# Optimization experiments

Measured on AMD Instinct MI355X. Metric: run time of the kernel, lower is better.

The kernel has to match this reference:

```python
import jax, jax.numpy as jnp
import numpy as np

B, N, C, K = 16, 2000, 4, 8
EPS = 1e-5


def setup_inputs() -> dict:
    key = jax.random.key(0)
    ks = jax.random.split(key, 10)
    def p(k, shape, s=0.1):
        return jax.random.normal(k, shape, jnp.float32) * s
    return {
        "data": jax.random.normal(ks[0], (B, 1, N, C), jnp.float32),
        "x": jax.random.normal(ks[1], (B, 1, N, 4), jnp.float32),
        "w1a": p(ks[2], (128, C)), "b1a": jnp.zeros((128,), jnp.float32),
        "w1b": p(ks[3], (128, 128)), "b1b": jnp.zeros((128,), jnp.float32),
        "w2": p(ks[4], (128, 2 * C + 2)), "b2": jnp.zeros((128,), jnp.float32),
        "res_wa": p(ks[5], (4, 128, 128)), "res_ba": jnp.zeros((4, 128), jnp.float32),
        "res_wb": p(ks[6], (4, 128, 128)), "res_bb": jnp.zeros((4, 128), jnp.float32),
        "wl": p(ks[7], (1, 128)), "bl": jnp.zeros((1,), jnp.float32),
    }


def conv1x1(t, w, b):
    # t: [B, Cin, H, W], w: [Cout, Cin]
    return jnp.einsum('bchw,oc->bohw', t, w) + b[None, :, None, None]


def bn(t):
    # training-mode BatchNorm2d, gamma=1 beta=0 (default init)
    m = jnp.mean(t, axis=(0, 2, 3), keepdims=True)
    v = jnp.var(t, axis=(0, 2, 3), keepdims=True)
    return (t - m) * jax.lax.rsqrt(v + EPS)


def instn(t):
    # InstanceNorm2d, affine=False
    m = jnp.mean(t, axis=(2, 3), keepdims=True)
    v = jnp.var(t, axis=(2, 3), keepdims=True)
    return (t - m) * jax.lax.rsqrt(v + EPS)


def res_block(t, wa, ba, wb, bb):
    h = jax.nn.relu(bn(instn(conv1x1(t, wa, ba))))
    h = bn(instn(conv1x1(h, wb, bb)))
    return jax.nn.relu(h + t)


def knn_idx(f, k):
    # f: [B, D, N]; negative squared distance, top-(k+1), drop self
    xx = jnp.sum(f * f, axis=1)                        # [B, N]
    inner = jnp.einsum('bdn,bdm->bnm', f, f)           # [B, N, N]
    pd = 2.0 * inner - xx[:, :, None] - xx[:, None, :]
    idx = jax.lax.top_k(pd, k + 1)[1]                  # [B, N, k+1]
    return idx[:, :, 1:]


def graph_feature(f, idx):
    # f: [B, D, N], idx: [B, N, k] -> [B, 2D, N, k]
    xf = jnp.transpose(f, (0, 2, 1))                   # [B, N, D]
    nb = jax.vmap(lambda a, i: a[i])(xf, idx)          # [B, N, k, D]
    xt = xf[:, :, None, :]
    gf = jnp.concatenate([jnp.broadcast_to(xt, nb.shape), xt - nb], axis=-1)
    return jnp.transpose(gf, (0, 3, 1, 2))


def reference(data, x, w1a, b1a, w1b, b1b, w2, b2,
              res_wa, res_ba, res_wb, res_bb, wl, bl):
    n = data.shape[2]
    t = jnp.transpose(data, (0, 3, 2, 1))              # [B, C, N, 1]

    # self_attention
    h = conv1x1(t, w1a, b1a)
    h = jax.nn.relu(bn(h))
    h = conv1x1(h, w1b, b1b)[..., 0]                   # [B, 128, N]
    h = h / (jnp.linalg.norm(h, axis=1, keepdims=True) + 1e-5)
    A_rowsum = jnp.einsum('bcn,bcm->bm', h, h)         # sum_i A[i, j]
    D = (A_rowsum - 1.0) / n                           # [B, N] (eye subtraction)
    feat = jnp.concatenate(
        [t, jax.nn.relu(jnp.tanh(D))[:, None, :, None]], axis=1)  # [B, C+1, N, 1]

    f = feat[..., 0]                                   # [B, C+1, N]
    idx = knn_idx(f, K)
    g = graph_feature(f, idx)                          # [B, 2C+2, N, K]

    out = jax.nn.relu(bn(conv1x1(g, w2, b2)))          # [B, 128, N, K]
    out = jnp.max(out, axis=-1, keepdims=True)         # [B, 128, N, 1]

    for i in range(4):
        out = res_block(out, res_wa[i], res_ba[i], res_wb[i], res_bb[i])

    logit = conv1x1(out, wl, bl)[:, 0, :, 0]           # [B, N]

    # weighted 8-point
    weights = jax.nn.relu(jnp.tanh(logit))             # [B, N]
    xp = jnp.transpose(x[:, 0], (0, 2, 1))             # [B, 4, N]
    ones = jnp.ones_like(xp[:, 0])
    X = jnp.stack([xp[:, 2] * xp[:, 0], xp[:, 2] * xp[:, 1], xp[:, 2],
                   xp[:, 3] * xp[:, 0], xp[:, 3] * xp[:, 1], xp[:, 3],
                   xp[:, 0], xp[:, 1], ones], axis=1)  # [B, 9, N]
    X = jnp.transpose(X, (0, 2, 1))                    # [B, N, 9]
    XwX = jnp.einsum('bnp,bnq->bpq', X, weights[:, :, None] * X)  # [B, 9, 9]
    _, v = jnp.linalg.eigh(XwX)                        # ascending eigvals
    e_hat = v[:, :, 0]                                 # smallest-eig eigenvector
    e_hat = e_hat / jnp.linalg.norm(e_hat, axis=1, keepdims=True)

    return (D, logit, e_hat)
```

## Files before the change

kernel.cpp:

```cpp
#include <hip/hip_runtime.h>
#include <math.h>

#define BB 16
#define NN 2000
#define CH 128
#define KNN 8
#define JCH 8
#define JSZ 250

__device__ inline float wred(float v) {
    for (int off = 32; off > 0; off >>= 1) v += __shfl_down(v, off, 64);
    return v;
}

__global__ void k_conv1(const float* __restrict__ data, const float* __restrict__ w1a,
                        const float* __restrict__ b1a, float* __restrict__ c1) {
    int i = blockIdx.x * 256 + threadIdx.x;
    if (i >= BB * CH * NN) return;
    int n = i % NN;
    int rest = i / NN;
    int o = rest & 127;
    int b = rest >> 7;
    const float* dp = data + (b * NN + n) * 4;
    float acc = b1a[o];
    for (int c = 0; c < 4; ++c) acc += w1a[o * 4 + c] * dp[c];
    c1[i] = acc;
}

__global__ void k_chanstats(const float* __restrict__ src, float* __restrict__ chAB) {
    int o = blockIdx.x;
    int tid = threadIdx.x;
    float s = 0.f, ss = 0.f;
    for (int b = 0; b < BB; ++b) {
        const float* p = src + (b * CH + o) * NN;
        for (int n = tid; n < NN; n += 256) { float v = p[n]; s += v; ss += v * v; }
    }
    s = wred(s); ss = wred(ss);
    __shared__ float sh[8];
    int wid = tid >> 6, lane = tid & 63;
    if (lane == 0) { sh[wid] = s; sh[4 + wid] = ss; }
    __syncthreads();
    if (tid == 0) {
        float S0 = sh[0] + sh[1] + sh[2] + sh[3];
        float SS = sh[4] + sh[5] + sh[6] + sh[7];
        float m = S0 / (float)(BB * NN);
        float var = SS / (float)(BB * NN) - m * m;
        float a = rsqrtf(var + 1e-5f);
        chAB[o] = a;
        chAB[CH + o] = -m * a;
    }
}

__global__ __launch_bounds__(256) void k_gemm(const float* __restrict__ X, const float* __restrict__ W,
                                              const float* __restrict__ bias, float* __restrict__ Y,
                                              const float* __restrict__ ab, int mode) {
    int ot = blockIdx.x, by = blockIdx.y;
    int b = by >> 5, nt = by & 31;
    int n0 = nt * 64, o0 = ot * 64;
    int tid = threadIdx.x;
    int tx = tid & 15, ty = tid >> 4;
    __shared__ __align__(16) float Xs[32][64];
    __shared__ __align__(16) float Ws[32][68];
    float acc[4][4] = {};
    for (int jc = 0; jc < 4; ++jc) {
#pragma unroll
        for (int q = 0; q < 2; ++q) {
            int e4 = q * 256 + tid;
            int jj = e4 >> 4, nn4 = e4 & 15;
            int j = jc * 32 + jj;
            int n = n0 + nn4 * 4;
            float4 v = make_float4(0.f, 0.f, 0.f, 0.f);
            if (n < NN) {
                v = *(const float4*)&X[(b * CH + j) * NN + n];
                if (mode == 1) {
                    float a_ = ab[j], o_ = ab[CH + j];
                    v.x = fmaxf(a_ * v.x + o_, 0.f);
                    v.y = fmaxf(a_ * v.y + o_, 0.f);
                    v.z = fmaxf(a_ * v.z + o_, 0.f);
                    v.w = fmaxf(a_ * v.w + o_, 0.f);
                } else if (mode == 2) {
                    int bc = b * CH + j;
                    float a_ = ab[bc * 2], o_ = ab[bc * 2 + 1];
                    v.x = fmaxf(a_ * v.x + o_, 0.f);
                    v.y = fmaxf(a_ * v.y + o_, 0.f);
                    v.z = fmaxf(a_ * v.z + o_, 0.f);
                    v.w = fmaxf(a_ * v.w + o_, 0.f);
                }
            }
            *(float4*)&Xs[jj][nn4 * 4] = v;
        }
#pragma unroll
        for (int q = 0; q < 2; ++q) {
            int e4 = q * 256 + tid;
            int oo = e4 >> 3, jj4 = e4 & 7;
            float4 wv4 = *(const float4*)&W[(o0 + oo) * CH + jc * 32 + jj4 * 4];
            Ws[jj4 * 4 + 0][oo] = wv4.x;
            Ws[jj4 * 4 + 1][oo] = wv4.y;
            Ws[jj4 * 4 + 2][oo] = wv4.z;
            Ws[jj4 * 4 + 3][oo] = wv4.w;
        }
        __syncthreads();
        for (int jj = 0; jj < 32; ++jj) {
            float4 wv = *(const float4*)&Ws[jj][ty * 4];
            float4 xv = *(const float4*)&Xs[jj][tx * 4];
            float wva[4] = {wv.x, wv.y, wv.z, wv.w};
            float xva[4] = {xv.x, xv.y, xv.z, xv.w};
#pragma unroll
            for (int a = 0; a < 4; ++a)
#pragma unroll
                for (int bq = 0; bq < 4; ++bq) acc[a][bq] += wva[a] * xva[bq];
        }
        __syncthreads();
    }
    for (int a = 0; a < 4; ++a) {
        int o = o0 + ty * 4 + a;
        float bi = bias[o];
        for (int q = 0; q < 4; ++q) {
            int n = n0 + tx * 4 + q;
            if (n < NN) Y[(b * CH + o) * NN + n] = acc[a][q] + bi;
        }
    }
}

__global__ void k_invn(const float* __restrict__ h2, float* __restrict__ invn) {
    int b = blockIdx.x >> 3, chunk = blockIdx.x & 7;
    int n = chunk * 256 + threadIdx.x;
    if (n >= NN) return;
    float acc = 0.f;
    for (int c = 0; c < CH; ++c) { float v = h2[(b * CH + c) * NN + n]; acc += v * v; }
    invn[b * NN + n] = 1.f / (sqrtf(acc) + 1e-5f);
}

__global__ void k_S(const float* __restrict__ h2, const float* __restrict__ invn, float* __restrict__ Sv) {
    int row = blockIdx.x;
    int b = row >> 7;
    const float* p = h2 + row * NN;
    const float* iv = invn + b * NN;
    float s = 0.f;
    for (int n = threadIdx.x; n < NN; n += 256) s += p[n] * iv[n];
    s = wred(s);
    __shared__ float sh[4];
    int wid = threadIdx.x >> 6, lane = threadIdx.x & 63;
    if (lane == 0) sh[wid] = s;
    __syncthreads();
    if (threadIdx.x == 0) Sv[row] = sh[0] + sh[1] + sh[2] + sh[3];
}

__global__ void k_Df(const float* __restrict__ h2, const float* __restrict__ invn,
                     const float* __restrict__ Sv, const float* __restrict__ data,
                     float* __restrict__ outD, float* __restrict__ f5) {
    int b = blockIdx.x >> 3, chunk = blockIdx.x & 7;
    int n = chunk * 256 + threadIdx.x;
    if (n >= NN) return;
    float acc = 0.f;
    for (int c = 0; c < CH; ++c) acc += h2[(b * CH + c) * NN + n] * Sv[b * CH + c];
    float Ar = acc * invn[b * NN + n];
    float Dv = (Ar - 1.0f) / (float)NN;
    outD[b * NN + n] = Dv;
    const float* dp = data + (b * NN + n) * 4;
    for (int c = 0; c < 4; ++c) f5[(b * 5 + c) * NN + n] = dp[c];
    f5[(b * 5 + 4) * NN + n] = fmaxf(tanhf(Dv), 0.f);
}

__device__ __forceinline__ void cas_fj(float& da, int& ja, float& db, int& jb) {
    bool sw = db < da;
    float d0 = sw ? db : da;
    float d1 = sw ? da : db;
    int j0 = sw ? jb : ja;
    int j1 = sw ? ja : jb;
    da = d0; db = d1; ja = j0; jb = j1;
}

__global__ __launch_bounds__(256, 4) void k_knn_part(const float* __restrict__ f5,
                                                     float* __restrict__ pd, int* __restrict__ pj) {
    __shared__ float4 fs4[256];
    __shared__ float fs1[256];
    int jc = blockIdx.x, ic = blockIdx.y, b = blockIdx.z;
    int j0 = jc * JSZ;
    int tid = threadIdx.x;
    const float* fb = f5 + b * 5 * NN;
    if (tid < JSZ) {
        float4 v;
        v.x = fb[0 * NN + j0 + tid];
        v.y = fb[1 * NN + j0 + tid];
        v.z = fb[2 * NN + j0 + tid];
        v.w = fb[3 * NN + j0 + tid];
        fs4[tid] = v;
        fs1[tid] = fb[4 * NN + j0 + tid];
    } else {
        fs4[tid] = make_float4(1e18f, 1e18f, 1e18f, 1e18f);
        fs1[tid] = 1e18f;
    }
    __syncthreads();
    int i = ic * 256 + tid;
    if (i >= NN) return;
    float fi0 = fb[i], fi1 = fb[NN + i], fi2 = fb[2 * NN + i], fi3 = fb[3 * NN + i], fi4 = fb[4 * NN + i];
    const float DINF = __int_as_float(0x7f800000);
    float bd[8]; int bj[8];
#pragma unroll
    for (int q = 0; q < 8; ++q) { bd[q] = 1e30f; bj[q] = 0x7fffffff; }
    for (int g = 0; g < 256; g += 8) {
        float gd[8]; int gj[8];
#pragma unroll
        for (int k = 0; k < 8; ++k) {
            float4 fj = fs4[g + k];
            float f4 = fs1[g + k];
            float a0 = fi0 - fj.x, a1 = fi1 - fj.y, a2 = fi2 - fj.z, a3 = fi3 - fj.w, a4 = fi4 - f4;
            float dd = a0 * a0 + a1 * a1 + a2 * a2 + a3 * a3 + a4 * a4;
            int jj = j0 + g + k;
            gd[k] = (jj == i) ? DINF : dd;
            gj[k] = jj;
        }
        cas_fj(gd[0], gj[0], gd[1], gj[1]); cas_fj(gd[2], gj[2], gd[3], gj[3]);
        cas_fj(gd[4], gj[4], gd[5], gj[5]); cas_fj(gd[6], gj[6], gd[7], gj[7]);
        cas_fj(gd[0], gj[0], gd[2], gj[2]); cas_fj(gd[1], gj[1], gd[3], gj[3]);
        cas_fj(gd[4], gj[4], gd[6], gj[6]); cas_fj(gd[5], gj[5], gd[7], gj[7]);
        cas_fj(gd[1], gj[1], gd[2], gj[2]); cas_fj(gd[5], gj[5], gd[6], gj[6]);
        cas_fj(gd[0], gj[0], gd[4], gj[4]); cas_fj(gd[1], gj[1], gd[5], gj[5]);
        cas_fj(gd[2], gj[2], gd[6], gj[6]); cas_fj(gd[3], gj[3], gd[7], gj[7]);
        cas_fj(gd[2], gj[2], gd[4], gj[4]); cas_fj(gd[3], gj[3], gd[5], gj[5]);
        cas_fj(gd[1], gj[1], gd[2], gj[2]); cas_fj(gd[3], gj[3], gd[4], gj[4]);
        cas_fj(gd[5], gj[5], gd[6], gj[6]);
#pragma unroll
        for (int q = 0; q < 8; ++q) {
            float yd = gd[7 - q]; int yj = gj[7 - q];
            bool kp = bd[q] < yd;
            bd[q] = kp ? bd[q] : yd;
            bj[q] = kp ? bj[q] : yj;
        }
        cas_fj(bd[0], bj[0], bd[4], bj[4]); cas_fj(bd[1], bj[1], bd[5], bj[5]);
        cas_fj(bd[2], bj[2], bd[6], bj[6]); cas_fj(bd[3], bj[3], bd[7], bj[7]);
        cas_fj(bd[0], bj[0], bd[2], bj[2]); cas_fj(bd[1], bj[1], bd[3], bj[3]);
        cas_fj(bd[4], bj[4], bd[6], bj[6]); cas_fj(bd[5], bj[5], bd[7], bj[7]);
        cas_fj(bd[0], bj[0], bd[1], bj[1]); cas_fj(bd[2], bj[2], bd[3], bj[3]);
        cas_fj(bd[4], bj[4], bd[5], bj[5]); cas_fj(bd[6], bj[6], bd[7], bj[7]);
    }
    long base = ((long)(b * NN + i) * JCH + jc) * 8;
#pragma unroll
    for (int q = 0; q < 8; ++q) { pd[base + q] = bd[q]; pj[base + q] = bj[q]; }
}

__global__ __launch_bounds__(256) void k_knn_merge(const float* __restrict__ pd, const int* __restrict__ pj,
                                                   int* __restrict__ idxb) {
    int s = blockIdx.x * 256 + threadIdx.x;
    if (s >= BB * NN) return;
    const float* dl = pd + (long)s * JCH * 8;
    const int* jl = pj + (long)s * JCH * 8;
    int ptr[JCH];
#pragma unroll
    for (int c = 0; c < JCH; ++c) ptr[c] = 0;
    for (int q = 0; q < 8; ++q) {
        float best = 1e38f; int bestj = 0x7fffffff; int bc = 0;
#pragma unroll
        for (int c = 0; c < JCH; ++c) {
            if (ptr[c] < 8) {
                float d = dl[c * 8 + ptr[c]];
                int j = jl[c * 8 + ptr[c]];
                if (d < best || (d == best && j < bestj)) { best = d; bestj = j; bc = c; }
            }
        }
        idxb[s * 8 + q] = bestj;
        ++ptr[bc];
    }
}

__global__ __launch_bounds__(128) void k_gstats(const float* __restrict__ f5, const int* __restrict__ idxb,
                                                double* __restrict__ gacc) {
    int s = blockIdx.x * 128 + threadIdx.x;
    float acc[65];
#pragma unroll
    for (int q = 0; q < 65; ++q) acc[q] = 0.f;
    if (s < BB * NN) {
        int b = s / NN, n = s - b * NN;
        float fo[5];
#pragma unroll
        for (int c = 0; c < 5; ++c) fo[c] = f5[(b * 5 + c) * NN + n];
        float sd[5] = {0, 0, 0, 0, 0};
        float sdd[15];
#pragma unroll
        for (int q = 0; q < 15; ++q) sdd[q] = 0.f;
        for (int k = 0; k < 8; ++k) {
            int j = idxb[s * 8 + k];
            float df[5];
#pragma unroll
            for (int c = 0; c < 5; ++c) df[c] = fo[c] - f5[(b * 5 + c) * NN + j];
#pragma unroll
            for (int c = 0; c < 5; ++c) sd[c] += df[c];
            int t = 0;
#pragma unroll
            for (int c = 0; c < 5; ++c)
#pragma unroll
                for (int d2 = c; d2 < 5; ++d2) { sdd[t] += df[c] * df[d2]; ++t; }
        }
#pragma unroll
        for (int c = 0; c < 5; ++c) { acc[c] = 8.f * fo[c]; acc[5 + c] = sd[c]; }
        int t = 10, sc = 0;
        for (int p = 0; p < 10; ++p)
            for (int q = p; q < 10; ++q) {
                float v;
                if (q < 5) v = 8.f * fo[p] * fo[q];
                else if (p < 5) v = fo[p] * sd[q - 5];
                else { v = sdd[sc]; ++sc; }
                acc[t++] = v;
            }
    }
#pragma unroll 1
    for (int q = 0; q < 65; ++q) {
        float v = acc[q];
        for (int off = 32; off > 0; off >>= 1) v += __shfl_down(v, off, 64);
        acc[q] = v;
    }
    __shared__ float sh[2][65];
    int lane = threadIdx.x & 63, wid = threadIdx.x >> 6;
    if (lane == 0) {
        for (int q = 0; q < 65; ++q) sh[wid][q] = acc[q];
    }
    __syncthreads();
    if (threadIdx.x < 65) {
        float tot = sh[0][threadIdx.x] + sh[1][threadIdx.x];
        atomicAdd(&gacc[threadIdx.x], (double)tot);
    }
}

__global__ void k_gfinal(const double* __restrict__ gacc, const float* __restrict__ w2,
                         const float* __restrict__ b2, float* __restrict__ g2ab) {
    int o = threadIdx.x;
    if (o >= 128) return;
    double inv = 1.0 / (double)(BB * NN * 8);
    double Wr[10];
    for (int c = 0; c < 10; ++c) Wr[c] = (double)w2[o * 10 + c];
    double gm[10];
    for (int c = 0; c < 10; ++c) gm[c] = gacc[c] * inv;
    double b0 = (double)b2[o];
    double mean = b0;
    for (int c = 0; c < 10; ++c) mean += Wr[c] * gm[c];
    double e2 = b0 * b0 + 2.0 * b0 * (mean - b0);
    int t = 10;
    for (int p = 0; p < 10; ++p)
        for (int q = p; q < 10; ++q) {
            double G = gacc[t] * inv; ++t;
            double contrib = Wr[p] * Wr[q] * G;
            e2 += (p == q) ? contrib : 2.0 * contrib;
        }
    double var = e2 - mean * mean;
    double a = 1.0 / sqrt(var + 1e-5);
    g2ab[o] = (float)a;
    g2ab[128 + o] = (float)(-mean * a);
}

__global__ __launch_bounds__(256) void k_graphconv(const float* __restrict__ f5, const int* __restrict__ idxb,
                                                   const float* __restrict__ w2, const float* __restrict__ b2,
                                                   const float* __restrict__ g2ab, float* __restrict__ x0) {
    __shared__ float ws[1280], bs[128];
    __shared__ float fo_s[16][5], fnb_s[16][8][5];
    __shared__ int idxs[16][8];
    int b = blockIdx.x / 125, tile = blockIdx.x % 125;
    int nbase = tile * 16;
    int tid = threadIdx.x;
    for (int e = tid; e < 1280; e += 256) ws[e] = w2[e];
    if (tid < 128) bs[tid] = b2[tid];
    if (tid < 128) { int nn = tid >> 3, k = tid & 7; idxs[nn][k] = idxb[(b * NN + nbase + nn) * 8 + k]; }
    if (tid >= 128 && tid < 208) { int e = tid - 128; int nn = e / 5, c = e % 5; fo_s[nn][c] = f5[(b * 5 + c) * NN + nbase + nn]; }
    __syncthreads();
    for (int e = tid; e < 640; e += 256) {
        int nn = e / 40, r = e % 40, k = r / 5, c = r % 5;
        fnb_s[nn][k][c] = f5[(b * 5 + c) * NN + idxs[nn][k]];
    }
    __syncthreads();
    int nn = tid & 15, og = tid >> 4;
    float fo[5];
#pragma unroll
    for (int c = 0; c < 5; ++c) fo[c] = fo_s[nn][c];
    for (int oo = 0; oo < 8; ++oo) {
        int o = og * 8 + oo;
        float base = bs[o];
        float wn[5];
#pragma unroll
        for (int c = 0; c < 5; ++c) {
            float w1 = ws[o * 10 + c], w5 = ws[o * 10 + 5 + c];
            base += (w1 + w5) * fo[c];
            wn[c] = w5;
        }
        float mx = -1e30f;
        for (int k = 0; k < 8; ++k) {
            float v = base;
#pragma unroll
            for (int c = 0; c < 5; ++c) v -= wn[c] * fnb_s[nn][k][c];
            mx = fmaxf(mx, v);
        }
        float y = fmaxf(g2ab[o] * mx + g2ab[128 + o], 0.f);
        x0[(b * CH + o) * NN + nbase + nn] = y;
    }
}

__global__ void k_rowstats(const float* __restrict__ src, float* __restrict__ stats) {
    int row = blockIdx.x;
    const float* p = src + row * NN;
    float s = 0.f, ss = 0.f;
    for (int n = threadIdx.x; n < NN; n += 256) { float v = p[n]; s += v; ss += v * v; }
    s = wred(s); ss = wred(ss);
    __shared__ float sh[8];
    int wid = threadIdx.x >> 6, lane = threadIdx.x & 63;
    if (lane == 0) { sh[wid] = s; sh[4 + wid] = ss; }
    __syncthreads();
    if (threadIdx.x == 0) {
        float S0 = sh[0] + sh[1] + sh[2] + sh[3];
        float SS = sh[4] + sh[5] + sh[6] + sh[7];
        float m = S0 / (float)NN;
        float var = SS / (float)NN - m * m;
        stats[row * 2] = m;
        stats[row * 2 + 1] = var;
    }
}

__global__ void k_finalize(const float* __restrict__ stats, float* __restrict__ ab) {
    int c = threadIdx.x;
    if (c >= 128) return;
    float acc = 0.f;
    for (int b = 0; b < BB; ++b) { float var = stats[(b * CH + c) * 2 + 1]; acc += var / (var + 1e-5f); }
    float vc = acc / (float)BB;
    float sc = rsqrtf(vc + 1e-5f);
    for (int b = 0; b < BB; ++b) {
        float m = stats[(b * CH + c) * 2];
        float var = stats[(b * CH + c) * 2 + 1];
        float a = rsqrtf(var + 1e-5f) * sc;
        ab[(b * CH + c) * 2] = a;
        ab[(b * CH + c) * 2 + 1] = -m * a;
    }
}

__global__ void k_resadd(const float* __restrict__ Bm, const float* __restrict__ ab,
                         const float* __restrict__ x, float* __restrict__ y) {
    int i = blockIdx.x * 256 + threadIdx.x;
    if (i >= BB * CH * NN) return;
    int bc = i / NN;
    float v = ab[bc * 2] * Bm[i] + ab[bc * 2 + 1] + x[i];
    y[i] = fmaxf(v, 0.f);
}

__global__ void k_logit(const float* __restrict__ x4, const float* __restrict__ wl,
                        const float* __restrict__ bl, float* __restrict__ outLogit) {
    int b = blockIdx.x >> 3, chunk = blockIdx.x & 7;
    int n = chunk * 256 + threadIdx.x;
    if (n >= NN) return;
    float acc = 0.f;
    for (int c = 0; c < CH; ++c) acc += wl[c] * x4[(b * CH + c) * NN + n];
    outLogit[b * NN + n] = acc + bl[0];
}

__global__ __launch_bounds__(256) void k_xwx(const float* __restrict__ logit, const float* __restrict__ x_in,
                                             float* __restrict__ XwX) {
    int b = blockIdx.x;
    int tid = threadIdx.x;
    float a[45];
#pragma unroll
    for (int q = 0; q < 45; ++q) a[q] = 0.f;
    for (int n = tid; n < NN; n += 256) {
        float lg = logit[b * NN + n];
        float w = fmaxf(tanhf(lg), 0.f);
        const float* xp = x_in + (b * NN + n) * 4;
        float px = xp[0], py = xp[1], z = xp[2], wq = xp[3];
        float X9[9] = {z * px, z * py, z, wq * px, wq * py, wq, px, py, 1.f};
        int t = 0;
#pragma unroll
        for (int p = 0; p < 9; ++p) {
            float wp = w * X9[p];
#pragma unroll
            for (int q = p; q < 9; ++q) { a[t] += wp * X9[q]; ++t; }
        }
    }
#pragma unroll 1
    for (int q = 0; q < 45; ++q) {
        float v = a[q];
        for (int off = 32; off > 0; off >>= 1) v += __shfl_down(v, off, 64);
        a[q] = v;
    }
    __shared__ float sh[4][45];
    int lane = tid & 63, wid = tid >> 6;
    if (lane == 0) {
        for (int q = 0; q < 45; ++q) sh[wid][q] = a[q];
    }
    __syncthreads();
    if (tid < 45) XwX[b * 45 + tid] = sh[0][tid] + sh[1][tid] + sh[2][tid] + sh[3][tid];
}

__device__ __forceinline__ float lgetf(float reg, int i) {
    return __int_as_float(__builtin_amdgcn_readlane(__float_as_int(reg), i));
}
__device__ __forceinline__ float wsum64(float v) {
    for (int off = 32; off > 0; off >>= 1) v += __shfl_xor(v, off, 64);
    return v;
}

__device__ inline float slapy2_f(float x, float y) {
    float xa = fabsf(x), ya = fabsf(y);
    float w = fmaxf(xa, ya), z = fminf(xa, ya);
    if (z == 0.f) return w;
    float q = z / w;
    return w * sqrtf(1.f + q * q);
}

__device__ inline void slartg_f(float f, float g, float& c, float& s, float& r) {
    if (g == 0.f) { c = 1.f; s = 0.f; r = f; }
    else if (f == 0.f) { c = 0.f; s = (g > 0.f ? 1.f : -1.f); r = fabsf(g); }
    else {
        float d = sqrtf(f * f + g * g);
        c = fabsf(f) / d;
        r = (f >= 0.f) ? d : -d;
        s = g / r;
    }
}

__device__ void slaev2_f(float a, float b, float c, float& rt1, float& rt2, float& cs1, float& sn1) {
    float sm = a + c, df = a - c;
    float adf = fabsf(df), tb = b + b, ab = fabsf(tb);
    float acmx, acmn;
    if (fabsf(a) > fabsf(c)) { acmx = a; acmn = c; } else { acmx = c; acmn = a; }
    float rt;
    if (adf > ab) { float q = ab / adf; rt = adf * sqrtf(1.f + q * q); }
    else if (adf < ab) { float q = adf / ab; rt = ab * sqrtf(1.f + q * q); }
    else rt = ab * sqrtf(2.f);
    int sgn1;
    if (sm < 0.f) { rt1 = 0.5f * (sm - rt); sgn1 = -1; rt2 = (acmx / rt1) * acmn - (b / rt1) * b; }
    else if (sm > 0.f) { rt1 = 0.5f * (sm + rt); sgn1 = 1; rt2 = (acmx / rt1) * acmn - (b / rt1) * b; }
    else { rt1 = 0.5f * rt; rt2 = -0.5f * rt; sgn1 = 1; }
    float cs; int sgn2;
    if (df >= 0.f) { cs = df + rt; sgn2 = 1; } else { cs = df - rt; sgn2 = -1; }
    float acs = fabsf(cs);
    if (acs > ab) {
        float ct = -tb / cs;
        sn1 = 1.f / sqrtf(1.f + ct * ct);
        cs1 = ct * sn1;
    } else {
        if (ab == 0.f) { cs1 = 1.f; sn1 = 0.f; }
        else { float tn = -cs / tb; cs1 = 1.f / sqrtf(1.f + tn * tn); sn1 = tn * cs1; }
    }
    if (sgn1 == sgn2) { float tn = cs1; cs1 = -sn1; sn1 = tn; }
}

#define ROTLOG_MAX 2560

__global__ __launch_bounds__(64) void k_eigh(const float* __restrict__ XwX, float* __restrict__ out_e) {
    __shared__ float Am[81];
    __shared__ float rcl[ROTLOG_MAX], rsl[ROTLOG_MAX];
    __shared__ int rjl[ROTLOG_MAX];
    int bb = blockIdx.x;
    int lane = threadIdx.x;
#define AA(i, j) Am[(i) * 9 + (j)]
#define DGET(i) lgetf(dreg, (i))
#define DSET(i, v) do { float _v = (v); dreg = (lane == (i)) ? _v : dreg; } while (0)
#define EGET(i) lgetf(ereg, (i))
#define ESET(i, v) do { float _v = (v); ereg = (lane == (i)) ? _v : ereg; } while (0)
    {
        const float* src = XwX + bb * 45;
        for (int e2 = lane; e2 < 81; e2 += 64) {
            int r0 = e2 / 9, c0 = e2 % 9;
            int a0 = r0 < c0 ? r0 : c0, b0 = r0 < c0 ? c0 : r0;
            int t = a0 * 9 - (a0 * (a0 - 1)) / 2 + (b0 - a0);
            Am[e2] = src[t];
        }
    }
    __syncthreads();
    float dreg = 0.f, ereg = 0.f, treg = 0.f;
    int cnt = 0;
    for (int i = 0; i < 8; ++i) {
        float alpha = AA(i + 1, i);
        float xn2 = 0.f;
        for (int j = i + 2; j < 9; ++j) xn2 += AA(j, i) * AA(j, i);
        float taui;
        if (xn2 == 0.f) { taui = 0.f; ESET(i, alpha); }
        else {
            float xnorm = sqrtf(xn2);
            float beta = slapy2_f(alpha, xnorm);
            beta = (alpha >= 0.f) ? -beta : beta;
            taui = (beta - alpha) / beta;
            float scl = 1.f / (alpha - beta);
            for (int j = i + 2; j < 9; ++j) AA(j, i) *= scl;
            ESET(i, beta);
            float p[9], w[9];
            for (int j = i + 1; j < 9; ++j) {
                float acc = AA(j, i + 1);
                for (int k2 = i + 2; k2 < 9; ++k2) acc += AA(j, k2) * AA(k2, i);
                p[j] = taui * acc;
            }
            float dot = p[i + 1];
            for (int j = i + 2; j < 9; ++j) dot += p[j] * AA(j, i);
            float alpha2 = -0.5f * taui * dot;
            w[i + 1] = p[i + 1] + alpha2;
            for (int j = i + 2; j < 9; ++j) w[j] = p[j] + alpha2 * AA(j, i);
            for (int j = i + 1; j < 9; ++j) {
                float vj = (j == i + 1) ? 1.f : AA(j, i);
                for (int k2 = i + 1; k2 < 9; ++k2) {
                    float vk = (k2 == i + 1) ? 1.f : AA(k2, i);
                    float upd = AA(j, k2) - (vj * w[k2] + w[j] * vk);
                    if (lane == 0) AA(j, k2) = upd;
                }
            }
        }
        treg = (lane == i) ? taui : treg;
    }
    dreg = (lane < 9) ? Am[lane * 10] : 0.f;
    const float eps = 5.9604645e-08f;
    const float eps2 = 3.5527137e-15f;
    const float safmin = 1.17549435e-38f;
    const int n = 9;
    int nmaxit = n * 30, jtot = 0;
    int l1 = 0;
    while (l1 <= n - 1) {
        if (l1 > 0) ESET(l1 - 1, 0.f);
        int m = n - 1;
        for (int mm = l1; mm <= n - 2; ++mm) {
            float tst = fabsf(EGET(mm));
            if (tst == 0.f) { m = mm; break; }
            if (tst <= (sqrtf(fabsf(DGET(mm))) * sqrtf(fabsf(DGET(mm + 1)))) * eps) { ESET(mm, 0.f); m = mm; break; }
        }
        int l = l1, lsv = l, lend = m, lendsv = lend;
        l1 = m + 1;
        if (lend == l) continue;
        if (fabsf(DGET(lend)) < fabsf(DGET(l))) { lend = lsv; l = lendsv; }
        if (lend > l) {
            for (;;) {
                int m2 = lend;
                if (l != lend) {
                    for (int mm = l; mm <= lend - 1; ++mm) {
                        float em = EGET(mm);
                        float tst = em * em;
                        if (tst <= (eps2 * fabsf(DGET(mm))) * fabsf(DGET(mm + 1)) + safmin) { m2 = mm; break; }
                    }
                }
                if (m2 < lend) ESET(m2, 0.f);
                float p = DGET(l);
                if (m2 == l) { DSET(l, p); ++l; if (l <= lend) continue; else break; }
                if (m2 == l + 1) {
                    float rt1, rt2, c, s;
                    slaev2_f(DGET(l), EGET(l), DGET(l + 1), rt1, rt2, c, s);
                    if (lane == 0) { rcl[cnt] = c; rsl[cnt] = s; rjl[cnt] = l; }
                    ++cnt;
                    DSET(l, rt1); DSET(l + 1, rt2); ESET(l, 0.f); l += 2;
                    if (l <= lend) continue; else break;
                }
                if (jtot == nmaxit) break;
                ++jtot;
                float g = (DGET(l + 1) - p) / (2.f * EGET(l));
                float r = slapy2_f(g, 1.f);
                g = DGET(m2) - p + EGET(l) / (g + (g >= 0.f ? fabsf(r) : -fabsf(r)));
                float s = 1.f, c = 1.f;
                p = 0.f;
                for (int i = m2 - 1; i >= l; --i) {
                    float ei = EGET(i);
                    float f = s * ei, bq = c * ei;
                    slartg_f(g, f, c, s, r);
                    if (i != m2 - 1) ESET(i + 1, r);
                    g = DGET(i + 1) - p;
                    r = (DGET(i) - g) * s + 2.f * c * bq;
                    p = s * r;
                    DSET(i + 1, g + p);
                    g = c * r - bq;
                    if (lane == 0) { rcl[cnt] = c; rsl[cnt] = -s; rjl[cnt] = i; }
                    ++cnt;
                }
                DSET(l, DGET(l) - p);
                ESET(l, g);
            }
        } else {
            for (;;) {
                int m2 = lend;
                if (l != lend) {
                    for (int mm = l; mm >= lend + 1; --mm) {
                        float em = EGET(mm - 1);
                        float tst = em * em;
                        if (tst <= (eps2 * fabsf(DGET(mm))) * fabsf(DGET(mm - 1)) + safmin) { m2 = mm; break; }
                    }
                }
                if (m2 > lend) ESET(m2 - 1, 0.f);
                float p = DGET(l);
                if (m2 == l) { DSET(l, p); --l; if (l >= lend) continue; else break; }
                if (m2 == l - 1) {
                    float rt1, rt2, c, s;
                    slaev2_f(DGET(l - 1), EGET(l - 1), DGET(l), rt1, rt2, c, s);
                    if (lane == 0) { rcl[cnt] = c; rsl[cnt] = s; rjl[cnt] = l - 1; }
                    ++cnt;
                    DSET(l - 1, rt1); DSET(l, rt2); ESET(l - 1, 0.f); l -= 2;
                    if (l >= lend) continue; else break;
                }
                if (jtot == nmaxit) break;
                ++jtot;
                float g = (DGET(l - 1) - p) / (2.f * EGET(l - 1));
                float r = slapy2_f(g, 1.f);
                g = DGET(m2) - p + EGET(l - 1) / (g + (g >= 0.f ? fabsf(r) : -fabsf(r)));
                float s = 1.f, c = 1.f;
                p = 0.f;
                for (int i = m2; i <= l - 1; ++i) {
                    float ei = EGET(i);
                    float f = s * ei, bq = c * ei;
                    slartg_f(g, f, c, s, r);
                    if (i != m2) ESET(i - 1, r);
                    g = DGET(i) - p;
                    r = (DGET(i + 1) - g) * s + 2.f * c * bq;
                    p = s * r;
                    DSET(i, g + p);
                    g = c * r - bq;
                    if (lane == 0) { rcl[cnt] = c; rsl[cnt] = s; rjl[cnt] = i; }
                    ++cnt;
                }
                DSET(l, DGET(l) - p);
                ESET(l - 1, g);
            }
        }
    }
    __syncthreads();
    int permreg = lane;
    for (int ii = 1; ii < 9; ++ii) {
        int i = ii - 1, kk = i;
        float p = DGET(i);
        for (int j = ii; j < 9; ++j) {
            float dj = DGET(j);
            if (dj < p) { kk = j; p = dj; }
        }
        if (kk != i) {
            float di = DGET(i);
            DSET(kk, di);
            DSET(i, p);
            int pi = __builtin_amdgcn_readlane(permreg, i);
            int pk = __builtin_amdgcn_readlane(permreg, kk);
            permreg = (lane == i) ? pk : permreg;
            permreg = (lane == kk) ? pi : permreg;
        }
    }
    int kcol = __builtin_amdgcn_readlane(permreg, 0);
    float v0reg = (lane == kcol) ? 1.f : 0.f;
    for (int t = cnt - 1; t >= 0; --t) {
        float c = rcl[t], s = rsl[t];
        int j = rjl[t];
        float a = lgetf(v0reg, j);
        float b2 = lgetf(v0reg, j + 1);
        float nj = c * a - s * b2;
        float nj1 = s * a + c * b2;
        v0reg = (lane == j) ? nj : v0reg;
        v0reg = (lane == j + 1) ? nj1 : v0reg;
    }
    for (int i = 7; i >= 0; --i) {
        float ti = lgetf(treg, i);
        if (ti == 0.f) continue;
        float avi = (lane >= i + 2 && lane <= 8) ? Am[lane * 9 + i] : 0.f;
        float contrib = 0.f;
        if (lane == i + 1) contrib = v0reg;
        else if (lane >= i + 2 && lane <= 8) contrib = avi * v0reg;
        float dot = wsum64(contrib) * ti;
        if (lane == i + 1) v0reg -= dot;
        else if (lane >= i + 2 && lane <= 8) v0reg -= avi * dot;
    }
    float sq = (lane < 9) ? v0reg * v0reg : 0.f;
    float nrm = sqrtf(wsum64(sq));
    if (lane < 9) out_e[bb * 9 + lane] = v0reg / nrm;
#undef AA
#undef DGET
#undef DSET
#undef EGET
#undef ESET
}

extern "C" void kernel_launch(void* const* d_in, const int* in_sizes, int n_in,
                              void* d_out, int out_size, void* d_ws, size_t ws_size,
                              hipStream_t stream) {
    const float* data = (const float*)d_in[0];
    const float* x_in = (const float*)d_in[1];
    const float* w1a = (const float*)d_in[2];
    const float* b1a = (const float*)d_in[3];
    const float* w1b = (const float*)d_in[4];
    const float* b1b = (const float*)d_in[5];
    const float* w2 = (const float*)d_in[6];
    const float* b2 = (const float*)d_in[7];
    const float* res_wa = (const float*)d_in[8];
    const float* res_ba = (const float*)d_in[9];
    const float* res_wb = (const float*)d_in[10];
    const float* res_bb = (const float*)d_in[11];
    const float* wl = (const float*)d_in[12];
    const float* bl = (const float*)d_in[13];
    float* out = (float*)d_out;

    double* gacc = (double*)d_ws;
    float* xwx = (float*)((char*)d_ws + 1024);
    float* fbase = (float*)((char*)d_ws + 16384);
    float* big0 = fbase;
    float* big1 = big0 + BB * CH * NN;
    float* big2 = big1 + BB * CH * NN;
    float* tbuf = big2 + BB * CH * NN;
    float* f5 = tbuf + BB * 4 * NN;
    float* invn = f5 + BB * 5 * NN;
    float* Sv = invn + BB * NN;
    int* idxb = (int*)(Sv + BB * CH);
    float* chAB = (float*)(idxb + BB * NN * 8);
    float* stA = chAB + 256;
    float* abA = stA + BB * CH * 2;
    float* stB = abA + BB * CH * 2;
    float* abB = stB + BB * CH * 2;
    float* g2ab = abB + BB * CH * 2;
    float* knn_pd = big2;
    int* knn_pj = (int*)(big2 + BB * NN * JCH * 8);

    hipMemsetAsync(d_ws, 0, 1024, stream);

    k_conv1<<<16000, 256, 0, stream>>>(data, w1a, b1a, big0);
    k_chanstats<<<128, 256, 0, stream>>>(big0, chAB);
    k_gemm<<<dim3(2, 512), 256, 0, stream>>>(big0, w1b, b1b, big1, chAB, 1);
    k_invn<<<128, 256, 0, stream>>>(big1, invn);
    k_S<<<2048, 256, 0, stream>>>(big1, invn, Sv);
    k_Df<<<128, 256, 0, stream>>>(big1, invn, Sv, data, out, f5);
    k_knn_part<<<dim3(JCH, 8, BB), 256, 0, stream>>>(f5, knn_pd, knn_pj);
    k_knn_merge<<<125, 256, 0, stream>>>(knn_pd, knn_pj, idxb);
    k_gstats<<<250, 128, 0, stream>>>(f5, idxb, gacc);
    k_gfinal<<<1, 128, 0, stream>>>(gacc, w2, b2, g2ab);
    k_graphconv<<<2000, 256, 0, stream>>>(f5, idxb, w2, b2, g2ab, big0);

    float* xb = big0;
    float* hb = big1;
    for (int i = 0; i < 4; ++i) {
        k_gemm<<<dim3(2, 512), 256, 0, stream>>>(xb, res_wa + i * CH * CH, res_ba + i * CH, hb, nullptr, 0);
        k_rowstats<<<2048, 256, 0, stream>>>(hb, stA);
        k_finalize<<<1, 128, 0, stream>>>(stA, abA);
        k_gemm<<<dim3(2, 512), 256, 0, stream>>>(hb, res_wb + i * CH * CH, res_bb + i * CH, big2, abA, 2);
        k_rowstats<<<2048, 256, 0, stream>>>(big2, stB);
        k_finalize<<<1, 128, 0, stream>>>(stB, abB);
        k_resadd<<<16000, 256, 0, stream>>>(big2, abB, xb, hb);
        float* tmp = xb; xb = hb; hb = tmp;
    }

    k_logit<<<128, 256, 0, stream>>>(xb, wl, bl, out + BB * NN);
    k_xwx<<<16, 256, 0, stream>>>(out + BB * NN, x_in, xwx);
    k_eigh<<<16, 64, 0, stream>>>(xwx, out + 2 * BB * NN);
}
```

Measured before the change: 744.8 us.

## Vectorize data loads with float4 and fix tridiagonalization shared-memory races

The 1x1 conv and the D/feature kernel now read the 4-channel input and the conv weights with single float4 loads instead of scalar loops. The Householder tridiagonalization in the eigen-solver kernel is unrolled and now stages column scaling and rank-2 updates in registers. Lane 0 writes them back between barriers, which removes read/write races on the shared matrix. The added syncthreads cost a little, but the eigensolver runs on tiny 9x9 matrices, so the overall effect is likely small.

```diff
diff --git a/kernel.cpp b/kernel.cpp
--- a/kernel.cpp
+++ b/kernel.cpp
@@ -21,9 +21,13 @@
     int rest = i / NN;
     int o = rest & 127;
     int b = rest >> 7;
-    const float* dp = data + (b * NN + n) * 4;
+    const float4 d4 = *(const float4*)(data + (b * NN + n) * 4);
+    const float4 w4 = *(const float4*)(w1a + o * 4);
     float acc = b1a[o];
-    for (int c = 0; c < 4; ++c) acc += w1a[o * 4 + c] * dp[c];
+    acc += w4.x * d4.x;
+    acc += w4.y * d4.y;
+    acc += w4.z * d4.z;
+    acc += w4.w * d4.w;
     c1[i] = acc;
 }
 
@@ -157,8 +161,11 @@
     float Ar = acc * invn[b * NN + n];
     float Dv = (Ar - 1.0f) / (float)NN;
     outD[b * NN + n] = Dv;
-    const float* dp = data + (b * NN + n) * 4;
-    for (int c = 0; c < 4; ++c) f5[(b * 5 + c) * NN + n] = dp[c];
+    const float4 d4 = *(const float4*)(data + (b * NN + n) * 4);
+    f5[(b * 5 + 0) * NN + n] = d4.x;
+    f5[(b * 5 + 1) * NN + n] = d4.y;
+    f5[(b * 5 + 2) * NN + n] = d4.z;
+    f5[(b * 5 + 3) * NN + n] = d4.w;
     f5[(b * 5 + 4) * NN + n] = fmaxf(tanhf(Dv), 0.f);
 }
 
@@ -563,9 +570,11 @@
     __syncthreads();
     float dreg = 0.f, ereg = 0.f, treg = 0.f;
     int cnt = 0;
+#pragma unroll
     for (int i = 0; i < 8; ++i) {
         float alpha = AA(i + 1, i);
         float xn2 = 0.f;
+#pragma unroll
         for (int j = i + 2; j < 9; ++j) xn2 += AA(j, i) * AA(j, i);
         float taui;
         if (xn2 == 0.f) { taui = 0.f; ESET(i, alpha); }
@@ -575,30 +584,54 @@
             beta = (alpha >= 0.f) ? -beta : beta;
             taui = (beta - alpha) / beta;
             float scl = 1.f / (alpha - beta);
-            for (int j = i + 2; j < 9; ++j) AA(j, i) *= scl;
+            float colv[9];
+#pragma unroll
+            for (int j = i + 2; j < 9; ++j) colv[j] = AA(j, i) * scl;
+            __syncthreads();
+            if (lane == 0) {
+#pragma unroll
+                for (int j = i + 2; j < 9; ++j) AA(j, i) = colv[j];
+            }
+            __syncthreads();
             ESET(i, beta);
             float p[9], w[9];
+#pragma unroll
             for (int j = i + 1; j < 9; ++j) {
                 float acc = AA(j, i + 1);
+#pragma unroll
                 for (int k2 = i + 2; k2 < 9; ++k2) acc += AA(j, k2) * AA(k2, i);
                 p[j] = taui * acc;
             }
             float dot = p[i + 1];
+#pragma unroll
             for (int j = i + 2; j < 9; ++j) dot += p[j] * AA(j, i);
             float alpha2 = -0.5f * taui * dot;
             w[i + 1] = p[i + 1] + alpha2;
+#pragma unroll
             for (int j = i + 2; j < 9; ++j) w[j] = p[j] + alpha2 * AA(j, i);
+            float updv[9][9];
+#pragma unroll
             for (int j = i + 1; j < 9; ++j) {
                 float vj = (j == i + 1) ? 1.f : AA(j, i);
+#pragma unroll
                 for (int k2 = i + 1; k2 < 9; ++k2) {
                     float vk = (k2 == i + 1) ? 1.f : AA(k2, i);
-                    float upd = AA(j, k2) - (vj * w[k2] + w[j] * vk);
-                    if (lane == 0) AA(j, k2) = upd;
+                    updv[j][k2] = AA(j, k2) - (vj * w[k2] + w[j] * vk);
                 }
             }
+            __syncthreads();
+            if (lane == 0) {
+#pragma unroll
+                for (int j = i + 1; j < 9; ++j)
+#pragma unroll
+                    for (int k2 = i + 1; k2 < 9; ++k2)
+                        AA(j, k2) = updv[j][k2];
+            }
+            __syncthreads();
         }
         treg = (lane == i) ? taui : treg;
     }
+    __syncthreads();
     dreg = (lane < 9) ? Am[lane * 10] : 0.f;
     const float eps = 5.9604645e-08f;
     const float eps2 = 3.5527137e-15f;
```

New measurement: 719.0 us. 1.04x faster.
